# Optimization experiments

Hardware: AMD Instinct MI355X
Metric: run time of the kernel (lower is better)

The kernel has to match this reference:

```python
import jax, jax.numpy as jnp
import numpy as np

H = 512          # lstm_hidden_size
NUM_OPS = 8
NUM_NODES = 4
TEMP = 5.0
TANH_C = 2.5
B = 4096
NUM_STEPS = 16   # 8 lstm steps x 2 decisions (node, op)


def setup_inputs() -> dict:
    key = jax.random.key(0)
    ks = jax.random.split(key, 20)
    u = lambda k, s: jax.random.uniform(k, s, jnp.float32, -0.1, 0.1)
    inp = {}
    # embedding: torch default init N(0,1)
    inp["emb"] = jax.random.normal(ks[0], (NUM_OPS + 1, H), jnp.float32)
    # LSTM (single layer), torch gate order i,f,g,o; init U(-0.1,0.1), bias 0
    inp["w_ih"] = u(ks[1], (4 * H, H))
    inp["w_hh"] = u(ks[2], (4 * H, H))
    inp["b_ih"] = jnp.zeros((4 * H,), jnp.float32)
    inp["b_hh"] = jnp.zeros((4 * H,), jnp.float32)
    # node-predecessor decoders: widths 2,3,4,5 (one per intermediate node)
    inp["wn2"] = u(ks[3], (2, H)); inp["bn2"] = jnp.zeros((2,), jnp.float32)
    inp["wn3"] = u(ks[4], (3, H)); inp["bn3"] = jnp.zeros((3,), jnp.float32)
    inp["wn4"] = u(ks[5], (4, H)); inp["bn4"] = jnp.zeros((4,), jnp.float32)
    inp["wn5"] = u(ks[6], (5, H)); inp["bn5"] = jnp.zeros((5,), jnp.float32)
    # op decoders: one [NUM_OPS, H] decoder per intermediate node
    inp["wop"] = u(ks[7], (NUM_NODES, NUM_OPS, H))
    inp["bop"] = jnp.zeros((NUM_NODES, NUM_OPS), jnp.float32)
    # Gumbel noise for multinomial sampling via Gumbel-max (padded to width 8)
    un = jax.random.uniform(ks[8], (NUM_STEPS, B, NUM_OPS), jnp.float32,
                            minval=1e-6, maxval=1.0 - 1e-6)
    inp["gumbel"] = -jnp.log(-jnp.log(un))
    inp["batch_size"] = B
    return inp


def _lstm_step(x, h, c, w_ih, w_hh, b_ih, b_hh):
    gates = x @ w_ih.T + h @ w_hh.T + b_ih + b_hh   # [B, 4H]
    i, f, g, o = jnp.split(gates, 4, axis=-1)
    i = jax.nn.sigmoid(i); f = jax.nn.sigmoid(f)
    g = jnp.tanh(g);       o = jax.nn.sigmoid(o)
    c = f * c + i * g
    h = o * jnp.tanh(c)
    return h, c


def _decide(logits, g):
    # logits: [B, k], g: [B, k] gumbel noise -> sample ~ softmax(logits)
    logp = jax.nn.log_softmax(logits, axis=-1)
    probs = jnp.exp(logp)
    action = jnp.argmax(logits + g, axis=-1)                     # [B]
    sel = jnp.take_along_axis(logp, action[:, None], 1)[:, 0]     # [B]
    ent = -(logp * probs).sum(-1)                                 # [B]
    return action, sel, ent


def reference(emb, w_ih, w_hh, b_ih, b_hh,
              wn2, bn2, wn3, bn3, wn4, bn4, wn5, bn5,
              wop, bop, gumbel, batch_size):
    node_dec = [(wn2, bn2), (wn3, bn3), (wn4, bn4), (wn5, bn5)]
    h = jnp.zeros((batch_size, H), emb.dtype)
    c = jnp.zeros((batch_size, H), emb.dtype)
    inputs = jnp.zeros((batch_size,), jnp.int32)   # initial token 0
    actions, log_probs, entropies = [], [], []
    step = 0
    for i in range(NUM_NODES):
        wn, bn = node_dec[i]
        k = wn.shape[0]
        for _ in range(2):  # two (prev_node, op) edges per node, one lstm step each
            x = emb[inputs]                                   # [B, H]
            h, c = _lstm_step(x, h, c, w_ih, w_hh, b_ih, b_hh)
            # node-predecessor decision: temperature + tanh squashing
            nl = TANH_C * jnp.tanh((h @ wn.T + bn) / TEMP)    # [B, k]
            a, s, e = _decide(nl, gumbel[step, :, :k])
            actions.append(a); log_probs.append(s); entropies.append(e)
            step += 1
            # op decision: temperature only (no tanh in original code)
            ol = (h @ wop[i].T + bop[i]) / TEMP               # [B, NUM_OPS]
            a, s, e = _decide(ol, gumbel[step])
            actions.append(a); log_probs.append(s); entropies.append(e)
            step += 1
            inputs = a  # op action feeds the next lstm step
    return (jnp.stack(actions).astype(jnp.int32),   # [16, B]
            jnp.stack(log_probs),                   # [16, B]
            jnp.stack(entropies))                   # [16, B]
```

## Files before the change

kernel.cpp:

```cpp
#include <hip/hip_runtime.h>


constexpr int Bsz = 4096;
constexpr int Hsz = 512;
constexpr int G4H = 2048;

typedef unsigned short ushort_t;
using short8 = __attribute__((ext_vector_type(8))) short;
using f32x4 = __attribute__((ext_vector_type(4))) float;

__device__ __forceinline__ ushort_t f2bf_hi(float f) {
  unsigned u = __float_as_uint(f);
  u += 0x7FFF + ((u >> 16) & 1);
  return (ushort_t)(u >> 16);
}
__device__ __forceinline__ float bf2f(ushort_t h) {
  return __uint_as_float((unsigned)h << 16);
}
__device__ __forceinline__ float sigf(float x) {
  return 1.0f / (1.0f + expf(-x));
}

__device__ __forceinline__ void glds16(const void* gsrc, void* ldst) {
  __builtin_amdgcn_global_load_lds(
      (const __attribute__((address_space(1))) void*)gsrc,
      (__attribute__((address_space(3))) void*)ldst, 16, 0, 0);
}

__global__ __launch_bounds__(256) void setup_fused(
    const float* __restrict__ emb, const float* __restrict__ w_ih,
    const float* __restrict__ b_ih, const float* __restrict__ b_hh,
    const float* __restrict__ w_hh, float* __restrict__ Eperm,
    ushort_t* __restrict__ Wcat) {
  if (blockIdx.x < 4608) {
    const int lane = threadIdx.x & 63;
    const int wid = (blockIdx.x << 2) + (threadIdx.x >> 6);
    const int t = wid >> 11;
    const int col = wid & 2047;
    const float* er = emb + (size_t)t * Hsz + (lane << 3);
    const float* wr = w_ih + (size_t)col * Hsz + (lane << 3);
    float4 e0 = *(const float4*)(er);
    float4 e1 = *(const float4*)(er + 4);
    float4 w0 = *(const float4*)(wr);
    float4 w1 = *(const float4*)(wr + 4);
    float v = e0.x * w0.x + e0.y * w0.y + e0.z * w0.z + e0.w * w0.w +
              e1.x * w1.x + e1.y * w1.y + e1.z * w1.z + e1.w * w1.w;
#pragma unroll
    for (int off = 32; off > 0; off >>= 1) v += __shfl_xor(v, off, 64);
    if (lane == 0) {
      float val = v + b_ih[col] + b_hh[col];
      Eperm[(size_t)t * G4H + ((col & 511) << 2) + (col >> 9)] = val;
    }
  } else {
    const int b = blockIdx.x - 4608;
    const int ct = b >> 2;
    const int k = ((b & 3) << 8) + threadIdx.x;
    const int j = ct >> 2, g = ct & 3;
    const float* srcrow = w_hh + (size_t)(g * 512 + j) * Hsz;
    ushort_t out;
    if (k < 512) {
      out = f2bf_hi(srcrow[k]);
    } else {
      float x = srcrow[k - 512];
      ushort_t hi = f2bf_hi(x);
      out = f2bf_hi(x - bf2f(hi));
    }
    Wcat[(size_t)ct * 1536 + k] = out;
  }
}

template <int K>
__device__ __forceinline__ void decide_core(
    const float4 hv0, const float4 hv1, const int lane, const int r,
    const float* __restrict__ wn, const float* __restrict__ bn,
    const float* __restrict__ wopi, const float* __restrict__ bopi,
    const float* __restrict__ gum, float* __restrict__ oan,
    float* __restrict__ oao, float* __restrict__ oln, float* __restrict__ olo,
    float* __restrict__ oen, float* __restrict__ oeo,
    int* __restrict__ act_next, const int* __restrict__ cls_prev,
    int* __restrict__ cls_out) {
  float nl[K];
#pragma unroll
  for (int j = 0; j < K; ++j) {
    const float* w = wn + (size_t)j * Hsz;
    float4 w0 = *(const float4*)(w + (lane << 3));
    float4 w1 = *(const float4*)(w + (lane << 3) + 4);
    float v = hv0.x * w0.x + hv0.y * w0.y + hv0.z * w0.z + hv0.w * w0.w +
              hv1.x * w1.x + hv1.y * w1.y + hv1.z * w1.z + hv1.w * w1.w;
#pragma unroll
    for (int off = 32; off > 0; off >>= 1) v += __shfl_xor(v, off, 64);
    nl[j] = 2.5f * tanhf((v + bn[j]) / 5.0f);
  }
  float ol[8];
#pragma unroll
  for (int j = 0; j < 8; ++j) {
    const float* w = wopi + (size_t)j * Hsz;
    float4 w0 = *(const float4*)(w + (lane << 3));
    float4 w1 = *(const float4*)(w + (lane << 3) + 4);
    float v = hv0.x * w0.x + hv0.y * w0.y + hv0.z * w0.z + hv0.w * w0.w +
              hv1.x * w1.x + hv1.y * w1.y + hv1.z * w1.z + hv1.w * w1.w;
#pragma unroll
    for (int off = 32; off > 0; off >>= 1) v += __shfl_xor(v, off, 64);
    ol[j] = (v + bopi[j]) / 5.0f;
  }

  {
    const float* g = gum + (size_t)r * 8;
    float m = nl[0];
#pragma unroll
    for (int j = 1; j < K; ++j) m = fmaxf(m, nl[j]);
    float se = 0.0f;
#pragma unroll
    for (int j = 0; j < K; ++j) se += expf(nl[j] - m);
    float lse = logf(se);
    int a = 0;
    float best = nl[0] + g[0];
#pragma unroll
    for (int j = 1; j < K; ++j) {
      float v = nl[j] + g[j];
      if (v > best) { best = v; a = j; }
    }
    float ent = 0.0f, sel = 0.0f;
#pragma unroll
    for (int j = 0; j < K; ++j) {
      float lp = nl[j] - m - lse;
      ent -= lp * expf(lp);
      if (j == a) sel = lp;
    }
    if (lane == 0) { oan[r] = (float)a; oln[r] = sel; oen[r] = ent; }
  }
  {
    const float* g = gum + (size_t)Bsz * 8 + (size_t)r * 8;
    float m = ol[0];
#pragma unroll
    for (int j = 1; j < 8; ++j) m = fmaxf(m, ol[j]);
    float se = 0.0f;
#pragma unroll
    for (int j = 0; j < 8; ++j) se += expf(ol[j] - m);
    float lse = logf(se);
    int a = 0;
    float best = ol[0] + g[0];
#pragma unroll
    for (int j = 1; j < 8; ++j) {
      float v = ol[j] + g[j];
      if (v > best) { best = v; a = j; }
    }
    float ent = 0.0f, sel = 0.0f;
#pragma unroll
    for (int j = 0; j < 8; ++j) {
      float lp = ol[j] - m - lse;
      ent -= lp * expf(lp);
      if (j == a) sel = lp;
    }
    if (lane == 0) {
      oao[r] = (float)a; olo[r] = sel; oeo[r] = ent;
      act_next[r] = a;
      if (cls_out) cls_out[r] = (cls_prev ? cls_prev[r] * 8 : 0) + a;
    }
  }
}

template <int K>
__device__ __forceinline__ void decide_core_s(
    const float* __restrict__ h8, const int lane, const int r,
    const float* __restrict__ wn, const float* __restrict__ bn,
    const float* __restrict__ wopi, const float* __restrict__ bopi,
    const float* __restrict__ gum, float* __restrict__ oan,
    float* __restrict__ oao, float* __restrict__ oln, float* __restrict__ olo,
    float* __restrict__ oen, float* __restrict__ oeo,
    int* __restrict__ act_next, const int* __restrict__ cls_prev,
    int* __restrict__ cls_out) {
  float nl[K];
#pragma unroll
  for (int j = 0; j < K; ++j) {
    const float* w = wn + (size_t)j * Hsz + lane;
    float v = 0.0f;
#pragma unroll
    for (int kk = 0; kk < 8; ++kk) v = fmaf(h8[kk], w[kk * 64], v);
#pragma unroll
    for (int off = 32; off > 0; off >>= 1) v += __shfl_xor(v, off, 64);
    nl[j] = 2.5f * tanhf((v + bn[j]) / 5.0f);
  }
  float ol[8];
#pragma unroll
  for (int j = 0; j < 8; ++j) {
    const float* w = wopi + (size_t)j * Hsz + lane;
    float v = 0.0f;
#pragma unroll
    for (int kk = 0; kk < 8; ++kk) v = fmaf(h8[kk], w[kk * 64], v);
#pragma unroll
    for (int off = 32; off > 0; off >>= 1) v += __shfl_xor(v, off, 64);
    ol[j] = (v + bopi[j]) / 5.0f;
  }

  {
    const float* g = gum + (size_t)r * 8;
    float m = nl[0];
#pragma unroll
    for (int j = 1; j < K; ++j) m = fmaxf(m, nl[j]);
    float se = 0.0f;
#pragma unroll
    for (int j = 0; j < K; ++j) se += expf(nl[j] - m);
    float lse = logf(se);
    int a = 0;
    float best = nl[0] + g[0];
#pragma unroll
    for (int j = 1; j < K; ++j) {
      float v = nl[j] + g[j];
      if (v > best) { best = v; a = j; }
    }
    float ent = 0.0f, sel = 0.0f;
#pragma unroll
    for (int j = 0; j < K; ++j) {
      float lp = nl[j] - m - lse;
      ent -= lp * expf(lp);
      if (j == a) sel = lp;
    }
    if (lane == 0) { oan[r] = (float)a; oln[r] = sel; oen[r] = ent; }
  }
  {
    const float* g = gum + (size_t)Bsz * 8 + (size_t)r * 8;
    float m = ol[0];
#pragma unroll
    for (int j = 1; j < 8; ++j) m = fmaxf(m, ol[j]);
    float se = 0.0f;
#pragma unroll
    for (int j = 0; j < 8; ++j) se += expf(ol[j] - m);
    float lse = logf(se);
    int a = 0;
    float best = ol[0] + g[0];
#pragma unroll
    for (int j = 1; j < 8; ++j) {
      float v = ol[j] + g[j];
      if (v > best) { best = v; a = j; }
    }
    float ent = 0.0f, sel = 0.0f;
#pragma unroll
    for (int j = 0; j < 8; ++j) {
      float lp = ol[j] - m - lse;
      ent -= lp * expf(lp);
      if (j == a) sel = lp;
    }
    if (lane == 0) {
      oao[r] = (float)a; olo[r] = sel; oeo[r] = ent;
      act_next[r] = a;
      if (cls_out) cls_out[r] = (cls_prev ? cls_prev[r] * 8 : 0) + a;
    }
  }
}

template <int K>
__global__ __launch_bounds__(256) void decide_step(
    const float* __restrict__ h, const float* __restrict__ wn,
    const float* __restrict__ bn, const float* __restrict__ wopi,
    const float* __restrict__ bopi, const float* __restrict__ gum,
    float* __restrict__ oan, float* __restrict__ oao,
    float* __restrict__ oln, float* __restrict__ olo,
    float* __restrict__ oen, float* __restrict__ oeo,
    int* __restrict__ act_next, const int* __restrict__ hidx, int hmode,
    const int* __restrict__ cls_prev, int* __restrict__ cls_out) {
  const int lane = threadIdx.x & 63;
  const int r = (blockIdx.x << 2) + (threadIdx.x >> 6);
  const int idx = (hmode == 1) ? r : hidx[r];
  const float* hr = h + (size_t)idx * Hsz;
  const float4 hv0 = *(const float4*)(hr + (lane << 3));
  const float4 hv1 = *(const float4*)(hr + (lane << 3) + 4);
  decide_core<K>(hv0, hv1, lane, r, wn, bn, wopi, bopi, gum, oan, oao, oln,
                 olo, oen, oeo, act_next, cls_prev, cls_out);
}

__global__ __launch_bounds__(256) void decide0_step(
    const float* __restrict__ Eperm, const float* __restrict__ wn,
    const float* __restrict__ bn, const float* __restrict__ wopi,
    const float* __restrict__ bopi, const float* __restrict__ gum,
    float* __restrict__ oan, float* __restrict__ oao,
    float* __restrict__ oln, float* __restrict__ olo,
    float* __restrict__ oen, float* __restrict__ oeo,
    int* __restrict__ act_next, int* __restrict__ cls_out) {
  const int lane = threadIdx.x & 63;
  const int r = (blockIdx.x << 2) + (threadIdx.x >> 6);
  float h8[8];
#pragma unroll
  for (int kk = 0; kk < 8; ++kk) {
    float4 e = *(const float4*)&Eperm[(size_t)(((lane << 3) + kk) << 2)];
    float ig = sigf(e.x);
    float gg = tanhf(e.z);
    float og = sigf(e.w);
    float cn = ig * gg;
    h8[kk] = og * tanhf(cn);
  }
  float4 hv0 = {h8[0], h8[1], h8[2], h8[3]};
  float4 hv1 = {h8[4], h8[5], h8[6], h8[7]};
  decide_core<2>(hv0, hv1, lane, r, wn, bn, wopi, bopi, gum, oan, oao, oln,
                 olo, oen, oeo, act_next, nullptr, cls_out);
}

__global__ __launch_bounds__(256) void fused_step1(
    const float* __restrict__ Eperm, const float* __restrict__ w_hh,
    float* __restrict__ h2, float* __restrict__ c2) {
  const int lane = threadIdx.x & 63;
  const int j = (blockIdx.x << 2) + (threadIdx.x >> 6);
  float h8[8];
#pragma unroll
  for (int kk = 0; kk < 8; ++kk) {
    float4 e = *(const float4*)&Eperm[(size_t)(((lane << 3) + kk) << 2)];
    h8[kk] = sigf(e.w) * tanhf(sigf(e.x) * tanhf(e.z));
  }
  float v[4];
#pragma unroll
  for (int g = 0; g < 4; ++g) {
    const float* w = w_hh + (size_t)(g * 512 + j) * Hsz + (lane << 3);
    float4 w0 = *(const float4*)(w);
    float4 w1 = *(const float4*)(w + 4);
    v[g] = h8[0] * w0.x + h8[1] * w0.y + h8[2] * w0.z + h8[3] * w0.w +
           h8[4] * w1.x + h8[5] * w1.y + h8[6] * w1.z + h8[7] * w1.w;
  }
#pragma unroll
  for (int off = 32; off > 0; off >>= 1) {
#pragma unroll
    for (int g = 0; g < 4; ++g) v[g] += __shfl_xor(v[g], off, 64);
  }
  float4 e0 = *(const float4*)&Eperm[(size_t)(j << 2)];
  float c1j = sigf(e0.x) * tanhf(e0.z);
  if (lane < 8) {
    const int er = lane;
    float4 e = *(const float4*)&Eperm[(size_t)er * G4H + (j << 2)];
    float ig = sigf(v[0] + e.x);
    float fg = sigf(v[1] + e.y);
    float gg = tanhf(v[2] + e.z);
    float og = sigf(v[3] + e.w);
    float cn = fg * c1j + ig * gg;
    h2[er * Hsz + j] = og * tanhf(cn);
    c2[er * Hsz + j] = cn;
  }
}

__global__ __launch_bounds__(256) void fused_step2(
    const float* __restrict__ Eperm, const float* __restrict__ w_hh,
    const float* __restrict__ h2, const float* __restrict__ c2,
    float* __restrict__ h3, float* __restrict__ c3) {
  const int lane = threadIdx.x & 63;
  const int wid = (blockIdx.x << 2) + (threadIdx.x >> 6);
  const int gq = wid >> 9, j = wid & 511;
  const float* hr = h2 + (size_t)gq * Hsz + (lane << 3);
  float4 a0 = *(const float4*)(hr);
  float4 a1 = *(const float4*)(hr + 4);
  float v[4];
#pragma unroll
  for (int g = 0; g < 4; ++g) {
    const float* w = w_hh + (size_t)(g * 512 + j) * Hsz + (lane << 3);
    float4 w0 = *(const float4*)(w);
    float4 w1 = *(const float4*)(w + 4);
    v[g] = a0.x * w0.x + a0.y * w0.y + a0.z * w0.z + a0.w * w0.w +
           a1.x * w1.x + a1.y * w1.y + a1.z * w1.z + a1.w * w1.w;
  }
#pragma unroll
  for (int off = 32; off > 0; off >>= 1) {
#pragma unroll
    for (int g = 0; g < 4; ++g) v[g] += __shfl_xor(v[g], off, 64);
  }
  float cp = c2[(size_t)gq * Hsz + j];
  if (lane < 8) {
    const int er = lane;
    float4 e = *(const float4*)&Eperm[(size_t)er * G4H + (j << 2)];
    float ig = sigf(v[0] + e.x);
    float fg = sigf(v[1] + e.y);
    float gg = tanhf(v[2] + e.z);
    float og = sigf(v[3] + e.w);
    float cn = fg * cp + ig * gg;
    h3[(size_t)((gq << 3) + er) * Hsz + j] = og * tanhf(cn);
    c3[(size_t)((gq << 3) + er) * Hsz + j] = cn;
  }
}

template <int MODE>
__global__ __launch_bounds__(256) void gemm64ct(
    const float* __restrict__ A, const float* __restrict__ w_hh,
    const float* __restrict__ Eperm, const float* __restrict__ c_in,
    float* __restrict__ Gperm, float* __restrict__ h_o,
    float* __restrict__ c_o) {
  constexpr int LDA = 68;
  __shared__ float As[16 * LDA];
  __shared__ float Bs[16 * LDA];
  const int tid = threadIdx.x;
  const int bx = blockIdx.x & 31;
  const int by = blockIdx.x >> 5;
  const int r0 = by * 64, c0 = bx * 64;
  const int tx = tid & 15, ty = tid >> 4;
  const int lr = tid >> 2;
  const int lk = (tid & 3) << 2;
  const int ct = c0 + lr;
  const int brow = (ct & 3) * 512 + (ct >> 2);
  const float* Ar = A + (size_t)(r0 + lr) * Hsz;
  const float* Br = w_hh + (size_t)brow * Hsz;
  float acc[4][4];
#pragma unroll
  for (int i = 0; i < 4; ++i)
#pragma unroll
    for (int j = 0; j < 4; ++j) acc[i][j] = 0.0f;

  for (int k0 = 0; k0 < Hsz; k0 += 16) {
    float4 a = *(const float4*)(Ar + k0 + lk);
    float4 b = *(const float4*)(Br + k0 + lk);
    __syncthreads();
    As[(lk + 0) * LDA + lr] = a.x;
    As[(lk + 1) * LDA + lr] = a.y;
    As[(lk + 2) * LDA + lr] = a.z;
    As[(lk + 3) * LDA + lr] = a.w;
    Bs[(lk + 0) * LDA + lr] = b.x;
    Bs[(lk + 1) * LDA + lr] = b.y;
    Bs[(lk + 2) * LDA + lr] = b.z;
    Bs[(lk + 3) * LDA + lr] = b.w;
    __syncthreads();
#pragma unroll
    for (int kk = 0; kk < 16; ++kk) {
      float4 av = *(const float4*)&As[kk * LDA + (ty << 2)];
      float4 bv = *(const float4*)&Bs[kk * LDA + (tx << 2)];
      float avs[4] = {av.x, av.y, av.z, av.w};
      float bvs[4] = {bv.x, bv.y, bv.z, bv.w};
#pragma unroll
      for (int i = 0; i < 4; ++i)
#pragma unroll
        for (int j = 0; j < 4; ++j) acc[i][j] = fmaf(avs[i], bvs[j], acc[i][j]);
    }
  }
  const int jcol = (c0 >> 2) + tx;
  if (MODE == 0) {
#pragma unroll
    for (int i = 0; i < 4; ++i) {
      float4 o = {acc[i][0], acc[i][1], acc[i][2], acc[i][3]};
      *(float4*)&Gperm[(size_t)(r0 + (ty << 2) + i) * G4H + (jcol << 2)] = o;
    }
  } else {
#pragma unroll
    for (int i = 0; i < 4; ++i) {
      const int q = r0 + (ty << 2) + i;
      float cp = c_in[(size_t)q * Hsz + jcol];
#pragma unroll
      for (int er = 0; er < 8; ++er) {
        float4 e = *(const float4*)&Eperm[(size_t)er * G4H + (jcol << 2)];
        float ig = sigf(acc[i][0] + e.x);
        float fg = sigf(acc[i][1] + e.y);
        float gg = tanhf(acc[i][2] + e.z);
        float og = sigf(acc[i][3] + e.w);
        float cn = fg * cp + ig * gg;
        h_o[(size_t)((q << 3) + er) * Hsz + jcol] = og * tanhf(cn);
        c_o[(size_t)((q << 3) + er) * Hsz + jcol] = cn;
      }
    }
  }
}

__global__ __launch_bounds__(256) void decide4_fused(
    const float* __restrict__ Gperm, const float* __restrict__ Eperm,
    const float* __restrict__ c4, const int* __restrict__ cls,
    float* __restrict__ cF, ushort_t* __restrict__ Acat,
    const float* __restrict__ wn, const float* __restrict__ bn,
    const float* __restrict__ wopi, const float* __restrict__ bopi,
    const float* __restrict__ gum, float* __restrict__ oan,
    float* __restrict__ oao, float* __restrict__ oln, float* __restrict__ olo,
    float* __restrict__ oen, float* __restrict__ oeo,
    int* __restrict__ act) {
  const int lane = threadIdx.x & 63;
  const int r = (blockIdx.x << 2) + (threadIdx.x >> 6);
  const int q = cls[r];
  const int er = act[r];
  const float* Gr = Gperm + (size_t)q * G4H;
  const float* Er = Eperm + (size_t)er * G4H;
  float h8[8];
#pragma unroll
  for (int kk = 0; kk < 8; ++kk) {
    const int j = kk * 64 + lane;
    float4 g4 = *(const float4*)&Gr[j << 2];
    float4 e4 = *(const float4*)&Er[j << 2];
    float ig = sigf(g4.x + e4.x);
    float fg = sigf(g4.y + e4.y);
    float gg = tanhf(g4.z + e4.z);
    float og = sigf(g4.w + e4.w);
    float cn = fg * c4[(size_t)q * Hsz + j] + ig * gg;
    float hn = og * tanhf(cn);
    cF[(size_t)r * Hsz + j] = cn;
    h8[kk] = hn;
    ushort_t hi = f2bf_hi(hn);
    Acat[(size_t)r * 1024 + j] = hi;
    Acat[(size_t)r * 1024 + 512 + j] = f2bf_hi(hn - bf2f(hi));
  }
  decide_core_s<4>(h8, lane, r, wn, bn, wopi, bopi, gum, oan, oao, oln,
                   olo, oen, oeo, act, nullptr, nullptr);
}

__global__ __launch_bounds__(256) void gemm_bf16_lstm(
    const ushort_t* __restrict__ Acat, const ushort_t* __restrict__ Wcat,
    const float* __restrict__ Eperm, const int* __restrict__ act,
    float* __restrict__ cF, float* __restrict__ h_out,
    ushort_t* __restrict__ Aout) {
  __shared__ union {
    ushort_t P[2][4][128 * 32];
    float C[64 * 132];
  } sm;

  const int tid = threadIdx.x;
  const int wave = tid >> 6, lane = tid & 63;
  const int xcd = blockIdx.x & 7;
  const int i64 = blockIdx.x >> 3;
  const int by = ((xcd >> 1) << 3) + (i64 >> 3);
  const int bx = ((xcd & 1) << 3) + (i64 & 7);
  const int r0 = by * 128, c0 = bx * 128;
  const int wr = (wave >> 1) * 64, wc = (wave & 1) * 64;
  const int mrow = lane & 15, quad = lane >> 4;

  const int srow = lane >> 2;
  const int sk = (lane & 3) << 3;

  const ushort_t* sbase[8];
  int doff[8];
#pragma unroll
  for (int q = 0; q < 8; ++q) {
    const int g = (q << 2) + wave;
    const int panel = g >> 3;
    const int region = g & 7;
    const int row = region * 16 + srow;
    if (panel == 0)
      sbase[q] = Acat + (size_t)(r0 + row) * 1024 + sk;
    else if (panel == 1)
      sbase[q] = Acat + (size_t)(r0 + row) * 1024 + 512 + sk;
    else if (panel == 2)
      sbase[q] = Wcat + (size_t)(c0 + row) * 1536 + sk;
    else
      sbase[q] = Wcat + (size_t)(c0 + row) * 1536 + 512 + sk;
    doff[q] = panel * 8192 + region * 1024;
  }

  f32x4 acc[4][4];
#pragma unroll
  for (int i = 0; i < 4; ++i)
#pragma unroll
    for (int jt = 0; jt < 4; ++jt) acc[i][jt] = (f32x4){0.f, 0.f, 0.f, 0.f};

  auto stage = [&](int buf, int it) {
    const int ks = it << 5;
#pragma unroll
    for (int q = 0; q < 8; ++q)
      glds16(sbase[q] + ks, (char*)sm.P[0][0] + (buf << 15) + doff[q]);
  };

  stage(0, 0);
  __syncthreads();

  int cur = 0;
  for (int it = 0; it < 16; ++it) {
    if (it < 15) stage(cur ^ 1, it + 1);
    const ushort_t* AH = sm.P[cur][0];
    const ushort_t* AL = sm.P[cur][1];
    const ushort_t* BH = sm.P[cur][2];
    const ushort_t* BL = sm.P[cur][3];
    short8 ah[4], al[4], bh[4], bl[4];
#pragma unroll
    for (int i = 0; i < 4; ++i) {
      ah[i] = *(const short8*)&AH[(wr + i * 16 + mrow) * 32 + (quad << 3)];
      al[i] = *(const short8*)&AL[(wr + i * 16 + mrow) * 32 + (quad << 3)];
    }
#pragma unroll
    for (int jt = 0; jt < 4; ++jt) {
      bh[jt] = *(const short8*)&BH[(wc + jt * 16 + mrow) * 32 + (quad << 3)];
      bl[jt] = *(const short8*)&BL[(wc + jt * 16 + mrow) * 32 + (quad << 3)];
    }
#pragma unroll
    for (int i = 0; i < 4; ++i)
#pragma unroll
      for (int jt = 0; jt < 4; ++jt) {
        acc[i][jt] = __builtin_amdgcn_mfma_f32_16x16x32_bf16(
            ah[i], bh[jt], acc[i][jt], 0, 0, 0);
        acc[i][jt] = __builtin_amdgcn_mfma_f32_16x16x32_bf16(
            ah[i], bl[jt], acc[i][jt], 0, 0, 0);
        acc[i][jt] = __builtin_amdgcn_mfma_f32_16x16x32_bf16(
            al[i], bh[jt], acc[i][jt], 0, 0, 0);
      }
    __syncthreads();
    cur ^= 1;
  }

  const int jj = tid & 31;
  const int rbase = tid >> 5;
#pragma unroll
  for (int p = 0; p < 2; ++p) {
    __syncthreads();
    if ((wr >> 6) == p) {
#pragma unroll
      for (int i = 0; i < 4; ++i)
#pragma unroll
        for (int jt = 0; jt < 4; ++jt)
#pragma unroll
          for (int rg = 0; rg < 4; ++rg)
            sm.C[(i * 16 + quad * 4 + rg) * 132 + wc + jt * 16 + mrow] =
                acc[i][jt][rg];
    }
    __syncthreads();
#pragma unroll
    for (int rp = 0; rp < 8; ++rp) {
      const int rl = rbase * 8 + rp;
      const int grow = r0 + p * 64 + rl;
      float4 g4 = *(float4*)&sm.C[rl * 132 + jj * 4];
      const int a = act[grow];
      const int jglob = (c0 >> 2) + jj;
      float4 e4 = *(const float4*)&Eperm[(size_t)a * G4H + c0 + jj * 4];
      float iv = g4.x + e4.x, fv = g4.y + e4.y;
      float gv = g4.z + e4.z, ov = g4.w + e4.w;
      float ig = 1.0f / (1.0f + expf(-iv));
      float fg = 1.0f / (1.0f + expf(-fv));
      float gg = tanhf(gv);
      float og = 1.0f / (1.0f + expf(-ov));
      const size_t ci = (size_t)grow * Hsz + jglob;
      float cn = fg * cF[ci] + ig * gg;
      float hn = og * tanhf(cn);
      cF[ci] = cn;
      h_out[ci] = hn;
      ushort_t hi = f2bf_hi(hn);
      Aout[(size_t)grow * 1024 + jglob] = hi;
      Aout[(size_t)grow * 1024 + 512 + jglob] = f2bf_hi(hn - bf2f(hi));
    }
  }
}

extern "C" void kernel_launch(void* const* d_in, const int* in_sizes, int n_in,
                              void* d_out, int out_size, void* d_ws,
                              size_t ws_size, hipStream_t stream) {
  (void)in_sizes; (void)n_in; (void)out_size; (void)ws_size;
  const float* emb = (const float*)d_in[0];
  const float* w_ih = (const float*)d_in[1];
  const float* w_hh = (const float*)d_in[2];
  const float* b_ih = (const float*)d_in[3];
  const float* b_hh = (const float*)d_in[4];
  const float* wn[4] = {(const float*)d_in[5], (const float*)d_in[7],
                        (const float*)d_in[9], (const float*)d_in[11]};
  const float* bn[4] = {(const float*)d_in[6], (const float*)d_in[8],
                        (const float*)d_in[10], (const float*)d_in[12]};
  const float* wop = (const float*)d_in[13];
  const float* bop = (const float*)d_in[14];
  const float* gum = (const float*)d_in[15];

  float* ws = (float*)d_ws;
  float* Eperm = ws;             ws += 9 * G4H;
  float* h2 = ws;                ws += 8 * Hsz;
  float* c2 = ws;                ws += 8 * Hsz;
  float* h3 = ws;                ws += 64 * Hsz;
  float* c3 = ws;                ws += 64 * Hsz;
  float* h4 = ws;                ws += 512 * Hsz;
  float* c4 = ws;                ws += 512 * Hsz;
  float* Gperm = ws;
  ushort_t* AcatB = (ushort_t*)Gperm;
  ws += (8u << 20) / 4;
  ushort_t* AcatA = (ushort_t*)ws;      ws += (8u << 20) / 4;
  ushort_t* Wcat = (ushort_t*)ws;       ws += (6u << 20) / 4;
  float* hA = ws;                ws += (size_t)Bsz * Hsz;
  float* cF = ws;                ws += (size_t)Bsz * Hsz;
  int* act = (int*)ws;
  int* cls = act + Bsz;

  float* out = (float*)d_out;
  const size_t SZ = (size_t)16 * Bsz;

  auto outp = [&](int s, float*& oan, float*& oao, float*& oln, float*& olo,
                  float*& oen, float*& oeo, const float*& gn) {
    oan = out + (size_t)(2 * s) * Bsz;
    oao = out + (size_t)(2 * s + 1) * Bsz;
    oln = out + SZ + (size_t)(2 * s) * Bsz;
    olo = out + SZ + (size_t)(2 * s + 1) * Bsz;
    oen = out + 2 * SZ + (size_t)(2 * s) * Bsz;
    oeo = out + 2 * SZ + (size_t)(2 * s + 1) * Bsz;
    gn = gum + (size_t)(2 * s) * Bsz * 8;
  };

  auto decide = [&](int s, const float* h, int hmode, const int* hidx,
                    const int* cls_prev, int* cls_out) {
    const int i = s >> 1;
    float *oan, *oao, *oln, *olo, *oen, *oeo;
    const float* gn;
    outp(s, oan, oao, oln, olo, oen, oeo, gn);
    const float* wopi = wop + (size_t)i * 8 * Hsz;
    const float* bopi = bop + (size_t)i * 8;
    switch (i) {
      case 0:
        decide_step<2><<<Bsz / 4, 256, 0, stream>>>(h, wn[0], bn[0], wopi, bopi,
            gn, oan, oao, oln, olo, oen, oeo, act, hidx, hmode, cls_prev, cls_out);
        break;
      case 1:
        decide_step<3><<<Bsz / 4, 256, 0, stream>>>(h, wn[1], bn[1], wopi, bopi,
            gn, oan, oao, oln, olo, oen, oeo, act, hidx, hmode, cls_prev, cls_out);
        break;
      case 2:
        decide_step<4><<<Bsz / 4, 256, 0, stream>>>(h, wn[2], bn[2], wopi, bopi,
            gn, oan, oao, oln, olo, oen, oeo, act, hidx, hmode, cls_prev, cls_out);
        break;
      default:
        decide_step<5><<<Bsz / 4, 256, 0, stream>>>(h, wn[3], bn[3], wopi, bopi,
            gn, oan, oao, oln, olo, oen, oeo, act, hidx, hmode, cls_prev, cls_out);
        break;
    }
  };

  setup_fused<<<4608 + 8192, 256, 0, stream>>>(emb, w_ih, b_ih, b_hh, w_hh,
                                               Eperm, Wcat);

  {
    float *oan, *oao, *oln, *olo, *oen, *oeo;
    const float* gn;
    outp(0, oan, oao, oln, olo, oen, oeo, gn);
    decide0_step<<<Bsz / 4, 256, 0, stream>>>(Eperm, wn[0], bn[0], wop, bop,
        gn, oan, oao, oln, olo, oen, oeo, act, cls);
  }

  fused_step1<<<128, 256, 0, stream>>>(Eperm, w_hh, h2, c2);
  decide(1, h2, 2, cls, cls, cls);

  fused_step2<<<1024, 256, 0, stream>>>(Eperm, w_hh, h2, c2, h3, c3);
  decide(2, h3, 2, cls, cls, cls);

  gemm64ct<1><<<32, 256, 0, stream>>>(h3, w_hh, Eperm, c3, nullptr, h4, c4);
  decide(3, h4, 2, cls, nullptr, nullptr);

  gemm64ct<0><<<256, 256, 0, stream>>>(h4, w_hh, nullptr, nullptr, Gperm,
                                       nullptr, nullptr);
  {
    float *oan, *oao, *oln, *olo, *oen, *oeo;
    const float* gn;
    outp(4, oan, oao, oln, olo, oen, oeo, gn);
    decide4_fused<<<Bsz / 4, 256, 0, stream>>>(Gperm, Eperm, c4, cls, cF,
        AcatA, wn[2], bn[2], wop + (size_t)2 * 8 * Hsz, bop + 2 * 8, gn,
        oan, oao, oln, olo, oen, oeo, act);
  }

  ushort_t* ain = AcatA;
  ushort_t* aout = AcatB;
  for (int s = 5; s < 8; ++s) {
    gemm_bf16_lstm<<<512, 256, 0, stream>>>(ain, Wcat, Eperm, act, cF, hA, aout);
    decide(s, hA, 1, nullptr, nullptr, nullptr);
    ushort_t* t = ain; ain = aout; aout = t;
  }
}
```

Measured before the change: 402.4 us.

## Triple-buffer LDS in LSTM GEMM with fine-grained vmcnt waits

Changes the LSTM gate GEMM main loop from double-buffered staging with two full syncthreads per iteration to a three-stage LDS ring. Each iteration waits only for the oldest in-flight global-to-LDS loads via vmcnt, issues one barrier, then prefetches two tiles ahead while computing. This is meant to hide global load latency better and cut barrier stalls. In exchange, LDS use rises to 96KB per block, which may lower occupancy, and correctness now depends on the manual vmcnt counts matching the number of loads issued.

```diff
diff --git a/kernel.cpp b/kernel.cpp
--- a/kernel.cpp
+++ b/kernel.cpp
@@ -495,7 +495,7 @@
     float* __restrict__ cF, float* __restrict__ h_out,
     ushort_t* __restrict__ Aout) {
   __shared__ union {
-    ushort_t P[2][4][128 * 32];
+    ushort_t P[3][4][128 * 32];
     float C[64 * 132];
   } sm;
 
@@ -541,19 +541,14 @@
     const int ks = it << 5;
 #pragma unroll
     for (int q = 0; q < 8; ++q)
-      glds16(sbase[q] + ks, (char*)sm.P[0][0] + (buf << 15) + doff[q]);
+      glds16(sbase[q] + ks, (char*)sm.P[buf][0] + doff[q]);
   };
 
-  stage(0, 0);
-  __syncthreads();
-
-  int cur = 0;
-  for (int it = 0; it < 16; ++it) {
-    if (it < 15) stage(cur ^ 1, it + 1);
-    const ushort_t* AH = sm.P[cur][0];
-    const ushort_t* AL = sm.P[cur][1];
-    const ushort_t* BH = sm.P[cur][2];
-    const ushort_t* BL = sm.P[cur][3];
+  auto compute = [&](int buf) {
+    const ushort_t* AH = sm.P[buf][0];
+    const ushort_t* AL = sm.P[buf][1];
+    const ushort_t* BH = sm.P[buf][2];
+    const ushort_t* BL = sm.P[buf][3];
     short8 ah[4], al[4], bh[4], bl[4];
 #pragma unroll
     for (int i = 0; i < 4; ++i) {
@@ -576,9 +571,30 @@
         acc[i][jt] = __builtin_amdgcn_mfma_f32_16x16x32_bf16(
             al[i], bh[jt], acc[i][jt], 0, 0, 0);
       }
-    __syncthreads();
-    cur ^= 1;
-  }
+  };
+
+  stage(0, 0);
+  stage(1, 1);
+
+  int cons = 0, sb = 2;
+#pragma unroll 1
+  for (int it = 0; it < 14; ++it) {
+    asm volatile("s_waitcnt vmcnt(8)" ::: "memory");
+    __builtin_amdgcn_sched_barrier(0);
+    __builtin_amdgcn_s_barrier();
+    stage(sb, it + 2);
+    compute(cons);
+    cons = (cons == 2) ? 0 : cons + 1;
+    sb = (sb == 2) ? 0 : sb + 1;
+  }
+  asm volatile("s_waitcnt vmcnt(8)" ::: "memory");
+  __builtin_amdgcn_sched_barrier(0);
+  __builtin_amdgcn_s_barrier();
+  compute(2);
+  asm volatile("s_waitcnt vmcnt(0)" ::: "memory");
+  __builtin_amdgcn_sched_barrier(0);
+  __builtin_amdgcn_s_barrier();
+  compute(0);
 
   const int jj = tid & 31;
   const int rbase = tid >> 5;
```

After: 572.0 us. 1.42x slower.

## Split-K the small recurrent GEMMs to fill more compute units

Applied to the files above, without the earlier changes.

The step-3 recurrent GEMM, which ran on only 32 blocks, is split along K into 8 slices across 256 blocks. The partial sums go to a buffer, and a new reduction kernel applies the LSTM cell. The step-4 GEMM is split in two along K, and decide4_fused adds the two partials as it reads them. This raises parallelism on kernels that leave most CUs idle, at the cost of extra partial-sum traffic and one more kernel launch.

```diff
diff --git a/kernel.cpp b/kernel.cpp
--- a/kernel.cpp
+++ b/kernel.cpp
@@ -373,18 +373,18 @@
   }
 }
 
-template <int MODE>
-__global__ __launch_bounds__(256) void gemm64ct(
+template <int NRT, int SK>
+__global__ __launch_bounds__(256) void gemm64ct_sk(
     const float* __restrict__ A, const float* __restrict__ w_hh,
-    const float* __restrict__ Eperm, const float* __restrict__ c_in,
-    float* __restrict__ Gperm, float* __restrict__ h_o,
-    float* __restrict__ c_o) {
+    float* __restrict__ Gpart) {
+  constexpr int LOG = (NRT == 1) ? 0 : (NRT == 2) ? 1 : (NRT == 4) ? 2 : 3;
   constexpr int LDA = 68;
   __shared__ float As[16 * LDA];
   __shared__ float Bs[16 * LDA];
   const int tid = threadIdx.x;
   const int bx = blockIdx.x & 31;
-  const int by = blockIdx.x >> 5;
+  const int by = (blockIdx.x >> 5) & (NRT - 1);
+  const int s = blockIdx.x >> (5 + LOG);
   const int r0 = by * 64, c0 = bx * 64;
   const int tx = tid & 15, ty = tid >> 4;
   const int lr = tid >> 2;
@@ -399,7 +399,9 @@
 #pragma unroll
     for (int j = 0; j < 4; ++j) acc[i][j] = 0.0f;
 
-  for (int k0 = 0; k0 < Hsz; k0 += 16) {
+  const int kBeg = s * (Hsz / SK);
+  const int kEnd = kBeg + Hsz / SK;
+  for (int k0 = kBeg; k0 < kEnd; k0 += 16) {
     float4 a = *(const float4*)(Ar + k0 + lk);
     float4 b = *(const float4*)(Br + k0 + lk);
     __syncthreads();
@@ -425,40 +427,49 @@
     }
   }
   const int jcol = (c0 >> 2) + tx;
-  if (MODE == 0) {
-#pragma unroll
-    for (int i = 0; i < 4; ++i) {
-      float4 o = {acc[i][0], acc[i][1], acc[i][2], acc[i][3]};
-      *(float4*)&Gperm[(size_t)(r0 + (ty << 2) + i) * G4H + (jcol << 2)] = o;
-    }
-  } else {
-#pragma unroll
-    for (int i = 0; i < 4; ++i) {
-      const int q = r0 + (ty << 2) + i;
-      float cp = c_in[(size_t)q * Hsz + jcol];
-#pragma unroll
-      for (int er = 0; er < 8; ++er) {
-        float4 e = *(const float4*)&Eperm[(size_t)er * G4H + (jcol << 2)];
-        float ig = sigf(acc[i][0] + e.x);
-        float fg = sigf(acc[i][1] + e.y);
-        float gg = tanhf(acc[i][2] + e.z);
-        float og = sigf(acc[i][3] + e.w);
-        float cn = fg * cp + ig * gg;
-        h_o[(size_t)((q << 3) + er) * Hsz + jcol] = og * tanhf(cn);
-        c_o[(size_t)((q << 3) + er) * Hsz + jcol] = cn;
-      }
-    }
+#pragma unroll
+  for (int i = 0; i < 4; ++i) {
+    float4 o = {acc[i][0], acc[i][1], acc[i][2], acc[i][3]};
+    *(float4*)&Gpart[((size_t)(s * NRT * 64) + r0 + (ty << 2) + i) * G4H +
+                     (jcol << 2)] = o;
+  }
+}
+
+__global__ __launch_bounds__(256) void fused_step3red(
+    const float* __restrict__ Gpart, const float* __restrict__ Eperm,
+    const float* __restrict__ c3, float* __restrict__ h4,
+    float* __restrict__ c4) {
+  const int idx = blockIdx.x * 256 + threadIdx.x;
+  const int q = idx >> 9, j = idx & 511;
+  float4 g = {0.f, 0.f, 0.f, 0.f};
+#pragma unroll
+  for (int s = 0; s < 8; ++s) {
+    float4 p = *(const float4*)&Gpart[(size_t)(s * 64 + q) * G4H + (j << 2)];
+    g.x += p.x; g.y += p.y; g.z += p.z; g.w += p.w;
+  }
+  const float cp = c3[(size_t)q * Hsz + j];
+#pragma unroll
+  for (int er = 0; er < 8; ++er) {
+    float4 e = *(const float4*)&Eperm[(size_t)er * G4H + (j << 2)];
+    float ig = sigf(g.x + e.x);
+    float fg = sigf(g.y + e.y);
+    float gg = tanhf(g.z + e.z);
+    float og = sigf(g.w + e.w);
+    float cn = fg * cp + ig * gg;
+    h4[(size_t)((q << 3) + er) * Hsz + j] = og * tanhf(cn);
+    c4[(size_t)((q << 3) + er) * Hsz + j] = cn;
   }
 }
 
 __global__ __launch_bounds__(256) void decide4_fused(
-    const float* __restrict__ Gperm, const float* __restrict__ Eperm,
-    const float* __restrict__ c4, const int* __restrict__ cls,
-    float* __restrict__ cF, ushort_t* __restrict__ Acat,
-    const float* __restrict__ wn, const float* __restrict__ bn,
-    const float* __restrict__ wopi, const float* __restrict__ bopi,
-    const float* __restrict__ gum, float* __restrict__ oan,
-    float* __restrict__ oao, float* __restrict__ oln, float* __restrict__ olo,
+    const float* __restrict__ Gperm, const float* __restrict__ Gperm2,
+    const float* __restrict__ Eperm, const float* __restrict__ c4,
+    const int* __restrict__ cls, float* __restrict__ cF,
+    ushort_t* __restrict__ Acat, const float* __restrict__ wn,
+    const float* __restrict__ bn, const float* __restrict__ wopi,
+    const float* __restrict__ bopi, const float* __restrict__ gum,
+    float* __restrict__ oan, float* __restrict__ oao,
+    float* __restrict__ oln, float* __restrict__ olo,
     float* __restrict__ oen, float* __restrict__ oeo,
     int* __restrict__ act) {
   const int lane = threadIdx.x & 63;
@@ -466,17 +477,19 @@
   const int q = cls[r];
   const int er = act[r];
   const float* Gr = Gperm + (size_t)q * G4H;
+  const float* Gr2 = Gperm2 + (size_t)q * G4H;
   const float* Er = Eperm + (size_t)er * G4H;
   float h8[8];
 #pragma unroll
   for (int kk = 0; kk < 8; ++kk) {
     const int j = kk * 64 + lane;
     float4 g4 = *(const float4*)&Gr[j << 2];
+    float4 p4 = *(const float4*)&Gr2[j << 2];
     float4 e4 = *(const float4*)&Er[j << 2];
-    float ig = sigf(g4.x + e4.x);
-    float fg = sigf(g4.y + e4.y);
-    float gg = tanhf(g4.z + e4.z);
-    float og = sigf(g4.w + e4.w);
+    float ig = sigf(g4.x + p4.x + e4.x);
+    float fg = sigf(g4.y + p4.y + e4.y);
+    float gg = tanhf(g4.z + p4.z + e4.z);
+    float og = sigf(g4.w + p4.w + e4.w);
     float cn = fg * c4[(size_t)q * Hsz + j] + ig * gg;
     float hn = og * tanhf(cn);
     cF[(size_t)r * Hsz + j] = cn;
@@ -716,17 +729,18 @@
   fused_step2<<<1024, 256, 0, stream>>>(Eperm, w_hh, h2, c2, h3, c3);
   decide(2, h3, 2, cls, cls, cls);
 
-  gemm64ct<1><<<32, 256, 0, stream>>>(h3, w_hh, Eperm, c3, nullptr, h4, c4);
+  gemm64ct_sk<1, 8><<<32 * 8, 256, 0, stream>>>(h3, w_hh, Gperm);
+  fused_step3red<<<128, 256, 0, stream>>>(Gperm, Eperm, c3, h4, c4);
   decide(3, h4, 2, cls, nullptr, nullptr);
 
-  gemm64ct<0><<<256, 256, 0, stream>>>(h4, w_hh, nullptr, nullptr, Gperm,
-                                       nullptr, nullptr);
+  gemm64ct_sk<8, 2><<<32 * 8 * 2, 256, 0, stream>>>(h4, w_hh, Gperm);
   {
     float *oan, *oao, *oln, *olo, *oen, *oeo;
     const float* gn;
     outp(4, oan, oao, oln, olo, oen, oeo, gn);
-    decide4_fused<<<Bsz / 4, 256, 0, stream>>>(Gperm, Eperm, c4, cls, cF,
-        AcatA, wn[2], bn[2], wop + (size_t)2 * 8 * Hsz, bop + 2 * 8, gn,
+    decide4_fused<<<Bsz / 4, 256, 0, stream>>>(Gperm,
+        Gperm + (size_t)512 * G4H, Eperm, c4, cls, cF, AcatA, wn[2], bn[2],
+        wop + (size_t)2 * 8 * Hsz, bop + 2 * 8, gn,
         oan, oao, oln, olo, oen, oeo, act);
   }
 
```

Result: faster. 375.4 us, median of 2 (-6.7%).
